# Performance work log

Hardware: AMD Instinct MI355X
Metric: run time of the kernel (lower is better)

Reference implementation:

```python
import jax, jax.numpy as jnp
import numpy as np

# Sizes (see shape_source): N samples, D=Config.dim, H=D//2, E question types, C classes/type
N, D, H, E, C = 65536, 768, 384, 8, 8


def setup_inputs() -> dict:
    key = jax.random.key(0)
    k_x, k_t, k_w1, k_w2 = jax.random.split(key, 4)
    x = jax.random.normal(k_x, (N, D), dtype=jnp.float32)
    question_types = jax.random.randint(k_t, (N,), 0, E, dtype=jnp.int32)
    # Stacked per-type MLP head parameters (E experts)
    W1 = jax.random.normal(k_w1, (E, D, H), dtype=jnp.float32) * 0.02
    b1 = jnp.zeros((E, H), dtype=jnp.float32)
    W2 = jax.random.normal(k_w2, (E, H, C), dtype=jnp.float32) * 0.02
    b2 = jnp.zeros((E, C), dtype=jnp.float32)
    return {"x": x, "W1": W1, "b1": b1, "W2": W2, "b2": b2,
            "question_types": question_types}


def reference(x, W1, b1, W2, b2, question_types):
    # Per-sample routed 2-layer MLP head: logits_i = MLP_{type_i}(x_i).
    # Dropout is eval-mode identity. Dense-per-expert compute + mask select
    # (standard MoE reference; E is a small fixed loop, not a data-dim loop).
    n_experts = W1.shape[0]
    out = jnp.zeros((x.shape[0], W2.shape[-1]), dtype=x.dtype)
    for e in range(n_experts):
        h = jax.nn.relu(x @ W1[e] + b1[e])        # [N, H]
        logits = h @ W2[e] + b2[e]                # [N, C]
        out = jnp.where((question_types == e)[:, None], logits, out)
    return out
```

## Files before the change

kernel.cpp:

```cpp
#include <hip/hip_runtime.h>

typedef short s16x8 __attribute__((ext_vector_type(8)));
typedef float f32x4 __attribute__((ext_vector_type(4)));

#define N_SAMPLES 65536
#define DIM 768
#define HID 384
#define NEXP 8
#define NCLS 8

#define WS_CNT    0
#define WS_BUCKET 1024
#define WS_W1T    (WS_BUCKET + NEXP * N_SAMPLES * 4)

__device__ __forceinline__ unsigned short f2bf(float f) {
  union { float f; unsigned u; } v; v.f = f;
  unsigned r = v.u + 0x7fffu + ((v.u >> 16) & 1u);
  return (unsigned short)(r >> 16);
}

__device__ __forceinline__ short f2bf_fast(float f) {
  union { float f; unsigned u; } v; v.f = f;
  return (short)((v.u + 0x8000u) >> 16);
}

__device__ __forceinline__ unsigned cvt2(float a, float b) {
  union { float f; unsigned u; } ua, ub;
  ua.f = a; ub.f = b;
  return __builtin_amdgcn_perm(ub.u + 0x8000u, ua.u + 0x8000u, 0x07060302u);
}

__global__ void k_transpose_w1(const float* __restrict__ W1,
                               unsigned short* __restrict__ W1T,
                               int* __restrict__ cnt) {
  if (blockIdx.x == 0 && blockIdx.y == 0 && blockIdx.z == 0 &&
      threadIdx.y == 0 && threadIdx.x < NEXP)
    cnt[threadIdx.x] = 0;
  __shared__ float tile[32][33];
  const int e = blockIdx.z, k0 = blockIdx.x * 32, j0 = blockIdx.y * 32;
  const int tx = threadIdx.x, ty = threadIdx.y;
  const float* src = W1 + (size_t)e * DIM * HID;
#pragma unroll
  for (int i = 0; i < 32; i += 8)
    tile[ty + i][tx] = src[(size_t)(k0 + ty + i) * HID + j0 + tx];
  __syncthreads();
  unsigned short* dst = W1T + (size_t)e * HID * DIM;
#pragma unroll
  for (int i = 0; i < 32; i += 8)
    dst[(size_t)(j0 + ty + i) * DIM + k0 + tx] = f2bf(tile[tx][ty + i]);
}

__global__ void k_scatter(const int* __restrict__ qt, int* __restrict__ cnt,
                          int* __restrict__ bucket) {
  __shared__ int lcnt[NEXP], lbase[NEXP];
  const int t = threadIdx.x;
  const int i = blockIdx.x * 256 + t;
  if (t < NEXP) lcnt[t] = 0;
  __syncthreads();
  const int e = qt[i];
  const int rank = atomicAdd(&lcnt[e], 1);
  __syncthreads();
  if (t < NEXP) lbase[t] = atomicAdd(&cnt[t], lcnt[t]);
  __syncthreads();
  bucket[(size_t)e * N_SAMPLES + lbase[e] + rank] = i;
}

#define GLL16(g, l)                                                        \
  __builtin_amdgcn_global_load_lds(                                        \
      (__attribute__((address_space(1))) void*)(void*)(g),                 \
      (__attribute__((address_space(3))) void*)(l), 16, 0, 0)

#define GLLB(KS, BUF)                                                      \
  _Pragma("unroll") for (int rep = 0; rep < 6; ++rep)                      \
      GLL16(bp + (size_t)rep * 64 * DIM + (KS) * 32, &(BUF)[(rep * 256 + t) * 8]);

#define ASTORE(BUF, LO, HI)                                                \
  {                                                                        \
    unsigned p01 = cvt2((LO).x, (LO).y), p23 = cvt2((LO).z, (LO).w);       \
    unsigned p45 = cvt2((HI).x, (HI).y), p67 = cvt2((HI).z, (HI).w);       \
    uint4 pk = {p01, p23, p45, p67};                                       \
    *(uint4*)&(BUF)[ar * 40 + aq * 8] = pk;                                \
  }

#define COMPUTE(AS, BS)                                                    \
  {                                                                        \
    s16x8 bfr[6];                                                          \
    _Pragma("unroll") for (int ni = 0; ni < 6; ++ni)                       \
        bfr[ni] = *(const s16x8*)&(BS)[(wave * 96 + ni * 16 + lrow) * 32 + quad * 8]; \
    _Pragma("unroll") for (int mi = 0; mi < 4; ++mi) {                     \
      s16x8 afr = *(const s16x8*)&(AS)[(mi * 16 + lrow) * 40 + quad * 8];  \
      _Pragma("unroll") for (int ni = 0; ni < 6; ++ni)                     \
          acc[mi][ni] = __builtin_amdgcn_mfma_f32_16x16x32_bf16(           \
              afr, bfr[ni], acc[mi][ni], 0, 0, 0);                         \
    }                                                                      \
  }

__global__ __launch_bounds__(256, 2) void k_moe_gemm(
    const float* __restrict__ x, const unsigned short* __restrict__ W1T,
    const float* __restrict__ b1, const float* __restrict__ W2,
    const float* __restrict__ b2, const int* __restrict__ cnt,
    const int* __restrict__ bucket, float* __restrict__ out) {
  __shared__ __align__(16) short smem[29696];
  __shared__ __align__(16) short W2s[16 * 392];
  __shared__ float b1s[HID];
  __shared__ float b2s[NCLS];
  short* As0 = smem;
  short* As1 = smem + 2560;
  short* Bs0 = smem + 5120;
  short* Bs1 = smem + 17408;
  short* Hs  = smem;

  const int e = blockIdx.x;
  const int n_e = cnt[e];
  const int t = threadIdx.x;
  const int lane = t & 63;
  const int wave = t >> 6;
  const int lrow = lane & 15;
  const int quad = lane >> 4;
  const int ar = t >> 2;
  const int aq = t & 3;

  for (int j = t; j < HID; j += 256) {
    b1s[j] = b1[e * HID + j];
    const float* wr = W2 + ((size_t)e * HID + j) * NCLS;
#pragma unroll
    for (int c = 0; c < NCLS; ++c) W2s[c * 392 + j] = (short)f2bf(wr[c]);
#pragma unroll
    for (int c = NCLS; c < 16; ++c) W2s[c * 392 + j] = 0;
  }
  if (t < NCLS) b2s[t] = b2[e * NCLS + t];

  const unsigned short* bp = W1T + ((size_t)e * HID + (t >> 2)) * DIM + (t & 3) * 8;

  for (int rt = blockIdx.y; rt * 64 < n_e; rt += gridDim.y) {
    const int row0 = rt * 64;
    int slot = row0 + ar;
    if (slot >= n_e) slot = n_e - 1;
    const int aidx = bucket[(size_t)e * N_SAMPLES + slot];
    const float* ap = x + (size_t)aidx * DIM + aq * 8;

    f32x4 acc[4][6];
#pragma unroll
    for (int mi = 0; mi < 4; ++mi)
#pragma unroll
      for (int ni = 0; ni < 6; ++ni) acc[mi][ni] = (f32x4){0.f, 0.f, 0.f, 0.f};

    float4 a0lo = ((const float4*)ap)[0];
    float4 a0hi = ((const float4*)(ap + 4))[0];
    GLLB(0, Bs0)
    ASTORE(As0, a0lo, a0hi)
    float4 a1lo = ((const float4*)(ap + 32))[0];
    float4 a1hi = ((const float4*)(ap + 36))[0];

    for (int ks = 0; ks < 24; ks += 2) {
      __syncthreads();
      if (ks + 1 < 24) { GLLB(ks + 1, Bs1) ASTORE(As1, a1lo, a1hi) }
      if (ks + 2 < 24) {
        a0lo = ((const float4*)(ap + (ks + 2) * 32))[0];
        a0hi = ((const float4*)(ap + (ks + 2) * 32 + 4))[0];
      }
      COMPUTE(As0, Bs0)
      __syncthreads();
      if (ks + 2 < 24) { GLLB(ks + 2, Bs0) ASTORE(As0, a0lo, a0hi) }
      if (ks + 3 < 24) {
        a1lo = ((const float4*)(ap + (ks + 3) * 32))[0];
        a1hi = ((const float4*)(ap + (ks + 3) * 32 + 4))[0];
      }
      COMPUTE(As1, Bs1)
    }

    __syncthreads();

#pragma unroll
    for (int mi = 0; mi < 4; ++mi)
#pragma unroll
      for (int ni = 0; ni < 6; ++ni) {
        const int j = wave * 96 + ni * 16 + lrow;
        const float bias = b1s[j];
#pragma unroll
        for (int r = 0; r < 4; ++r) {
          float v = acc[mi][ni][r] + bias;
          v = v > 0.f ? v : 0.f;
          Hs[(mi * 16 + quad * 4 + r) * 392 + j] = f2bf_fast(v);
        }
      }
    __syncthreads();

    {
      f32x4 acc2 = (f32x4){0.f, 0.f, 0.f, 0.f};
#pragma unroll
      for (int kk = 0; kk < 12; ++kk) {
        s16x8 af = *(const s16x8*)&Hs[(wave * 16 + lrow) * 392 + kk * 32 + quad * 8];
        s16x8 bf = *(const s16x8*)&W2s[lrow * 392 + kk * 32 + quad * 8];
        acc2 = __builtin_amdgcn_mfma_f32_16x16x32_bf16(af, bf, acc2, 0, 0, 0);
      }
      if (lrow < NCLS) {
        const float bb = b2s[lrow];
#pragma unroll
        for (int r = 0; r < 4; ++r) {
          const int m = wave * 16 + quad * 4 + r;
          if (row0 + m < n_e) {
            const int oi = bucket[(size_t)e * N_SAMPLES + row0 + m];
            out[(size_t)oi * NCLS + lrow] = acc2[r] + bb;
          }
        }
      }
    }
    __syncthreads();
  }
}

extern "C" void kernel_launch(void* const* d_in, const int* in_sizes, int n_in,
                              void* d_out, int out_size, void* d_ws, size_t ws_size,
                              hipStream_t stream) {
  const float* x  = (const float*)d_in[0];
  const float* W1 = (const float*)d_in[1];
  const float* b1 = (const float*)d_in[2];
  const float* W2 = (const float*)d_in[3];
  const float* b2 = (const float*)d_in[4];
  const int* qt   = (const int*)d_in[5];
  float* out = (float*)d_out;
  char* ws = (char*)d_ws;

  int* cnt = (int*)(ws + WS_CNT);
  int* bucket = (int*)(ws + WS_BUCKET);
  unsigned short* W1T = (unsigned short*)(ws + WS_W1T);

  k_transpose_w1<<<dim3(24, 12, 8), dim3(32, 8), 0, stream>>>(W1, W1T, cnt);
  k_scatter<<<dim3(256), dim3(256), 0, stream>>>(qt, cnt, bucket);
  k_moe_gemm<<<dim3(8, 64), dim3(256), 0, stream>>>(x, W1T, b1, W2, b2, cnt, bucket, out);
}
```

Baseline: 349.1 us.

## Prepack W1 into MFMA fragment layout and load weights directly to registers

The W1 preprocessing kernel now writes bf16 weights already arranged in per-lane MFMA fragment order, so the GEMM loads B fragments straight from global memory into registers instead of staging them through LDS with global_load_lds. The MFMA operands are swapped so the accumulator layout lets the bias/ReLU epilogue write four packed bf16 values per store. Barriers become a custom LDS-only waitcnt+barrier, and LDS use shrinks. The cost is more register pressure, weight loads that are now exposed to global latency, and a barrier that only waits on LDS counters.

```diff
diff --git a/kernel.cpp b/kernel.cpp
--- a/kernel.cpp
+++ b/kernel.cpp
@@ -8,10 +8,12 @@
 #define HID 384
 #define NEXP 8
 #define NCLS 8
+#define JT 24
+#define KT 24
 
 #define WS_CNT    0
 #define WS_BUCKET 1024
-#define WS_W1T    (WS_BUCKET + NEXP * N_SAMPLES * 4)
+#define WS_W1F    (WS_BUCKET + NEXP * N_SAMPLES * 4)
 
 __device__ __forceinline__ unsigned short f2bf(float f) {
   union { float f; unsigned u; } v; v.f = f;
@@ -19,35 +21,30 @@
   return (unsigned short)(r >> 16);
 }
 
-__device__ __forceinline__ short f2bf_fast(float f) {
-  union { float f; unsigned u; } v; v.f = f;
-  return (short)((v.u + 0x8000u) >> 16);
-}
-
 __device__ __forceinline__ unsigned cvt2(float a, float b) {
   union { float f; unsigned u; } ua, ub;
   ua.f = a; ub.f = b;
   return __builtin_amdgcn_perm(ub.u + 0x8000u, ua.u + 0x8000u, 0x07060302u);
 }
 
-__global__ void k_transpose_w1(const float* __restrict__ W1,
-                               unsigned short* __restrict__ W1T,
-                               int* __restrict__ cnt) {
-  if (blockIdx.x == 0 && blockIdx.y == 0 && blockIdx.z == 0 &&
-      threadIdx.y == 0 && threadIdx.x < NEXP)
+#define LBAR asm volatile("s_waitcnt lgkmcnt(0)\n\ts_barrier" ::: "memory")
+
+__global__ void k_w1frag(const float* __restrict__ W1,
+                         unsigned short* __restrict__ W1F,
+                         int* __restrict__ cnt) {
+  if (blockIdx.x == 0 && blockIdx.y == 0 && threadIdx.x < NEXP)
     cnt[threadIdx.x] = 0;
-  __shared__ float tile[32][33];
-  const int e = blockIdx.z, k0 = blockIdx.x * 32, j0 = blockIdx.y * 32;
-  const int tx = threadIdx.x, ty = threadIdx.y;
-  const float* src = W1 + (size_t)e * DIM * HID;
-#pragma unroll
-  for (int i = 0; i < 32; i += 8)
-    tile[ty + i][tx] = src[(size_t)(k0 + ty + i) * HID + j0 + tx];
-  __syncthreads();
-  unsigned short* dst = W1T + (size_t)e * HID * DIM;
-#pragma unroll
-  for (int i = 0; i < 32; i += 8)
-    dst[(size_t)(j0 + ty + i) * DIM + k0 + tx] = f2bf(tile[tx][ty + i]);
+  const int e = blockIdx.x;
+  const int unit = blockIdx.y * 4 + (threadIdx.x >> 6);
+  const int lane = threadIdx.x & 63;
+  const int jt = unit / KT, kt = unit % KT;
+  const int j = jt * 16 + (lane & 15);
+  const int k0 = kt * 32 + (lane >> 4) * 8;
+  const float* src = W1 + ((size_t)e * DIM + k0) * HID + j;
+  s16x8 v;
+#pragma unroll
+  for (int i = 0; i < 8; ++i) v[i] = (short)f2bf(src[(size_t)i * HID]);
+  *(s16x8*)&W1F[(((size_t)e * JT * KT + unit) * 64 + lane) * 8] = v;
 }
 
 __global__ void k_scatter(const int* __restrict__ qt, int* __restrict__ cnt,
@@ -65,49 +62,38 @@
   bucket[(size_t)e * N_SAMPLES + lbase[e] + rank] = i;
 }
 
-#define GLL16(g, l)                                                        \
-  __builtin_amdgcn_global_load_lds(                                        \
-      (__attribute__((address_space(1))) void*)(void*)(g),                 \
-      (__attribute__((address_space(3))) void*)(l), 16, 0, 0)
-
-#define GLLB(KS, BUF)                                                      \
-  _Pragma("unroll") for (int rep = 0; rep < 6; ++rep)                      \
-      GLL16(bp + (size_t)rep * 64 * DIM + (KS) * 32, &(BUF)[(rep * 256 + t) * 8]);
-
-#define ASTORE(BUF, LO, HI)                                                \
-  {                                                                        \
-    unsigned p01 = cvt2((LO).x, (LO).y), p23 = cvt2((LO).z, (LO).w);       \
-    unsigned p45 = cvt2((HI).x, (HI).y), p67 = cvt2((HI).z, (HI).w);       \
-    uint4 pk = {p01, p23, p45, p67};                                       \
-    *(uint4*)&(BUF)[ar * 40 + aq * 8] = pk;                                \
-  }
-
-#define COMPUTE(AS, BS)                                                    \
-  {                                                                        \
-    s16x8 bfr[6];                                                          \
-    _Pragma("unroll") for (int ni = 0; ni < 6; ++ni)                       \
-        bfr[ni] = *(const s16x8*)&(BS)[(wave * 96 + ni * 16 + lrow) * 32 + quad * 8]; \
-    _Pragma("unroll") for (int mi = 0; mi < 4; ++mi) {                     \
-      s16x8 afr = *(const s16x8*)&(AS)[(mi * 16 + lrow) * 40 + quad * 8];  \
-      _Pragma("unroll") for (int ni = 0; ni < 6; ++ni)                     \
-          acc[mi][ni] = __builtin_amdgcn_mfma_f32_16x16x32_bf16(           \
-              afr, bfr[ni], acc[mi][ni], 0, 0, 0);                         \
-    }                                                                      \
-  }
+#define ALOAD(LO, HI, KS)                                   \
+  { const float4* p_ = (const float4*)(ap + (KS) * 32);     \
+    LO = p_[0]; HI = p_[1]; }
+
+#define ASTORE(BUF, LO, HI)                                               \
+  { unsigned q0 = cvt2((LO).x, (LO).y), q1 = cvt2((LO).z, (LO).w);        \
+    unsigned q2 = cvt2((HI).x, (HI).y), q3 = cvt2((HI).z, (HI).w);        \
+    uint4 pk_ = {q0, q1, q2, q3};                                         \
+    *(uint4*)&(BUF)[ar * 40 + aq * 8] = pk_; }
+
+#define WLOAD(DST, KS)                                                    \
+  _Pragma("unroll") for (int ni = 0; ni < 6; ++ni)                        \
+      DST[ni] = *(const s16x8*)(wfbase + ((size_t)ni * KT + (KS)) * 512);
+
+#define COMPUTE(AS, WF)                                                   \
+  { _Pragma("unroll") for (int mi = 0; mi < 4; ++mi) {                    \
+      s16x8 xfr = *(const s16x8*)&(AS)[(mi * 16 + lrow) * 40 + quad * 8]; \
+      _Pragma("unroll") for (int ni = 0; ni < 6; ++ni)                    \
+          acc[mi][ni] = __builtin_amdgcn_mfma_f32_16x16x32_bf16(          \
+              WF[ni], xfr, acc[mi][ni], 0, 0, 0); } }
 
 __global__ __launch_bounds__(256, 2) void k_moe_gemm(
-    const float* __restrict__ x, const unsigned short* __restrict__ W1T,
+    const float* __restrict__ x, const unsigned short* __restrict__ W1F,
     const float* __restrict__ b1, const float* __restrict__ W2,
     const float* __restrict__ b2, const int* __restrict__ cnt,
     const int* __restrict__ bucket, float* __restrict__ out) {
-  __shared__ __align__(16) short smem[29696];
+  __shared__ __align__(16) short smem[25088];
   __shared__ __align__(16) short W2s[16 * 392];
   __shared__ float b1s[HID];
   __shared__ float b2s[NCLS];
   short* As0 = smem;
   short* As1 = smem + 2560;
-  short* Bs0 = smem + 5120;
-  short* Bs1 = smem + 17408;
   short* Hs  = smem;
 
   const int e = blockIdx.x;
@@ -130,7 +116,8 @@
   }
   if (t < NCLS) b2s[t] = b2[e * NCLS + t];
 
-  const unsigned short* bp = W1T + ((size_t)e * HID + (t >> 2)) * DIM + (t & 3) * 8;
+  const unsigned short* wfbase =
+      W1F + ((size_t)(e * JT + wave * 6) * KT) * 512 + lane * 8;
 
   for (int rt = blockIdx.y; rt * 64 < n_e; rt += gridDim.y) {
     const int row0 = rt * 64;
@@ -145,46 +132,39 @@
 #pragma unroll
       for (int ni = 0; ni < 6; ++ni) acc[mi][ni] = (f32x4){0.f, 0.f, 0.f, 0.f};
 
-    float4 a0lo = ((const float4*)ap)[0];
-    float4 a0hi = ((const float4*)(ap + 4))[0];
-    GLLB(0, Bs0)
+    float4 a0lo, a0hi, a1lo, a1hi;
+    s16x8 wf0[6], wf1[6];
+    ALOAD(a0lo, a0hi, 0)
     ASTORE(As0, a0lo, a0hi)
-    float4 a1lo = ((const float4*)(ap + 32))[0];
-    float4 a1hi = ((const float4*)(ap + 36))[0];
+    ALOAD(a1lo, a1hi, 1)
+    WLOAD(wf0, 0)
+    LBAR;
 
     for (int ks = 0; ks < 24; ks += 2) {
-      __syncthreads();
-      if (ks + 1 < 24) { GLLB(ks + 1, Bs1) ASTORE(As1, a1lo, a1hi) }
-      if (ks + 2 < 24) {
-        a0lo = ((const float4*)(ap + (ks + 2) * 32))[0];
-        a0hi = ((const float4*)(ap + (ks + 2) * 32 + 4))[0];
+      if (ks + 1 < 24) { ASTORE(As1, a1lo, a1hi) WLOAD(wf1, ks + 1) }
+      if (ks + 2 < 24) ALOAD(a0lo, a0hi, ks + 2)
+      COMPUTE(As0, wf0)
+      LBAR;
+      if (ks + 2 < 24) { ASTORE(As0, a0lo, a0hi) WLOAD(wf0, ks + 2) }
+      if (ks + 3 < 24) ALOAD(a1lo, a1hi, ks + 3)
+      COMPUTE(As1, wf1)
+      LBAR;
+    }
+
+#pragma unroll
+    for (int mi = 0; mi < 4; ++mi)
+#pragma unroll
+      for (int ni = 0; ni < 6; ++ni) {
+        const int j = wave * 96 + ni * 16 + quad * 4;
+        const float4 bb = *(const float4*)&b1s[j];
+        float v0 = acc[mi][ni][0] + bb.x; v0 = v0 > 0.f ? v0 : 0.f;
+        float v1 = acc[mi][ni][1] + bb.y; v1 = v1 > 0.f ? v1 : 0.f;
+        float v2 = acc[mi][ni][2] + bb.z; v2 = v2 > 0.f ? v2 : 0.f;
+        float v3 = acc[mi][ni][3] + bb.w; v3 = v3 > 0.f ? v3 : 0.f;
+        uint2 pk = {cvt2(v0, v1), cvt2(v2, v3)};
+        *(uint2*)&Hs[(mi * 16 + lrow) * 392 + j] = pk;
       }
-      COMPUTE(As0, Bs0)
-      __syncthreads();
-      if (ks + 2 < 24) { GLLB(ks + 2, Bs0) ASTORE(As0, a0lo, a0hi) }
-      if (ks + 3 < 24) {
-        a1lo = ((const float4*)(ap + (ks + 3) * 32))[0];
-        a1hi = ((const float4*)(ap + (ks + 3) * 32 + 4))[0];
-      }
-      COMPUTE(As1, Bs1)
-    }
-
-    __syncthreads();
-
-#pragma unroll
-    for (int mi = 0; mi < 4; ++mi)
-#pragma unroll
-      for (int ni = 0; ni < 6; ++ni) {
-        const int j = wave * 96 + ni * 16 + lrow;
-        const float bias = b1s[j];
-#pragma unroll
-        for (int r = 0; r < 4; ++r) {
-          float v = acc[mi][ni][r] + bias;
-          v = v > 0.f ? v : 0.f;
-          Hs[(mi * 16 + quad * 4 + r) * 392 + j] = f2bf_fast(v);
-        }
-      }
-    __syncthreads();
+    LBAR;
 
     {
       f32x4 acc2 = (f32x4){0.f, 0.f, 0.f, 0.f};
@@ -206,7 +186,7 @@
         }
       }
     }
-    __syncthreads();
+    LBAR;
   }
 }
 
@@ -224,9 +204,9 @@
 
   int* cnt = (int*)(ws + WS_CNT);
   int* bucket = (int*)(ws + WS_BUCKET);
-  unsigned short* W1T = (unsigned short*)(ws + WS_W1T);
-
-  k_transpose_w1<<<dim3(24, 12, 8), dim3(32, 8), 0, stream>>>(W1, W1T, cnt);
+  unsigned short* W1F = (unsigned short*)(ws + WS_W1F);
+
+  k_w1frag<<<dim3(8, 144), dim3(256), 0, stream>>>(W1, W1F, cnt);
   k_scatter<<<dim3(256), dim3(256), 0, stream>>>(qt, cnt, bucket);
-  k_moe_gemm<<<dim3(8, 64), dim3(256), 0, stream>>>(x, W1T, b1, W2, b2, cnt, bucket, out);
-}
+  k_moe_gemm<<<dim3(8, 64), dim3(256), 0, stream>>>(x, W1F, b1, W2, b2, cnt, bucket, out);
+}
```

Measured after the change: 334.8 us. 1.04x faster.
